# Optimization experiments

Measured on AMD Instinct MI355X. Metric: run time of the kernel, lower is better.

The kernel has to match this reference:

```python
import jax, jax.numpy as jnp
import numpy as np

N = 100000
E = 1600000
D_IN = 128
H = 128
C = 3
EPS_BN = 1e-5
EPS_LN = 1e-5


def _gcn_conv(x, W, b, src, dst, ew, n):
    # PyG GCNConv: x' = D^{-1/2} (A + I) D^{-1/2} (x W) + b, self-loop weight 1
    x = x @ W
    loop = jnp.arange(n)
    src2 = jnp.concatenate([src, loop])
    dst2 = jnp.concatenate([dst, loop])
    ew2 = jnp.concatenate([ew, jnp.ones((n,), dtype=x.dtype)])
    deg = jax.ops.segment_sum(ew2, dst2, num_segments=n)
    dinv = jnp.where(deg > 0, jax.lax.rsqrt(jnp.maximum(deg, 1e-12)), 0.0)
    norm = dinv[src2] * ew2 * dinv[dst2]  # [E+N]
    msgs = x[src2] * norm[:, None]        # [E+N, H] gathered messages
    out = jax.ops.segment_sum(msgs, dst2, num_segments=n)
    return out + b


def setup_inputs() -> dict:
    key = jax.random.key(0)
    ks = jax.random.split(key, 16)
    def lin(k, i, o):
        s = 1.0 / np.sqrt(i)
        k1, k2 = jax.random.split(k)
        return (jax.random.uniform(k1, (i, o), jnp.float32, -s, s),
                jax.random.uniform(k2, (o,), jnp.float32, -s, s))
    x = jax.random.normal(ks[0], (N, D_IN), jnp.float32)
    edge_index = jax.random.randint(ks[1], (2, E), 0, N, jnp.int64)
    edge_attr = jax.random.uniform(ks[2], (E, 1), jnp.float32)
    W_pre, b_pre = lin(ks[3], D_IN, H)
    W1, b1 = lin(ks[4], H, H)
    W2, b2 = lin(ks[5], H, H)
    Wc1, bc1 = lin(ks[6], H, H)
    Wc2, bc2 = lin(ks[7], H, C)
    return {
        "x": x, "edge_index": edge_index, "edge_attr": edge_attr,
        "W_pre": W_pre, "b_pre": b_pre,
        "bn_gamma": jnp.ones((H,), jnp.float32), "bn_beta": jnp.zeros((H,), jnp.float32),
        "bn_mean": jnp.zeros((H,), jnp.float32), "bn_var": jnp.ones((H,), jnp.float32),
        "W1": W1, "b1": b1, "W2": W2, "b2": b2,
        "Wc1": Wc1, "bc1": bc1,
        "ln_g": jnp.ones((H,), jnp.float32), "ln_b": jnp.zeros((H,), jnp.float32),
        "Wc2": Wc2, "bc2": bc2,
    }


def reference(x, edge_index, edge_attr, W_pre, b_pre, bn_gamma, bn_beta, bn_mean, bn_var,
              W1, b1, W2, b2, Wc1, bc1, ln_g, ln_b, Wc2, bc2):
    src, dst = edge_index[0], edge_index[1]
    ew = edge_attr.squeeze()
    n = x.shape[0]
    # input_preprocess: Linear -> BatchNorm1d (eval: running stats) -> ReLU (dropout=identity)
    h = x @ W_pre + b_pre
    h = (h - bn_mean) * jax.lax.rsqrt(bn_var + EPS_BN) * bn_gamma + bn_beta
    h = jax.nn.relu(h)
    residual = h
    # conv layer 1 (+ ReLU, dropout identity in eval)
    h = jax.nn.relu(_gcn_conv(h, W1, b1, src, dst, ew, n))
    # conv layer 2 (last: no activation)
    h = _gcn_conv(h, W2, b2, src, dst, ew, n)
    h = h + residual  # shapes match
    # classifier: Linear -> LayerNorm -> ReLU -> (dropout) -> Linear
    z = h @ Wc1 + bc1
    mu = jnp.mean(z, axis=-1, keepdims=True)
    var = jnp.mean((z - mu) ** 2, axis=-1, keepdims=True)
    z = (z - mu) * jax.lax.rsqrt(var + EPS_LN) * ln_g + ln_b
    z = jax.nn.relu(z)
    return z @ Wc2 + bc2
```

## Files before the change

### kernel.cpp

```cpp
#include <hip/hip_runtime.h>
#include <hip/hip_bf16.h>

typedef __bf16 bf16_t;
typedef bf16_t bf16x8 __attribute__((ext_vector_type(8)));
typedef float f32x4 __attribute__((ext_vector_type(4)));
typedef float f32x2 __attribute__((ext_vector_type(2)));

#define EPS_BN 1e-5f
#define EPS_LN 1e-5f
#define SLOTS 32
#define WSCALE 32767.f
#define WINV (1.f / 32767.f)
#define RNODES 448
#define OV_CAP 16384
#define OVA_CAP 65536

__device__ __forceinline__ float blo(unsigned u) { return __uint_as_float(u << 16); }
__device__ __forceinline__ float bhi(unsigned u) { return __uint_as_float(u & 0xFFFF0000u); }
__device__ __forceinline__ f32x2 f8lo(unsigned u) { return __builtin_amdgcn_cvt_pk_f32_fp8((int)u, false); }
__device__ __forceinline__ f32x2 f8hi(unsigned u) { return __builtin_amdgcn_cvt_pk_f32_fp8((int)u, true); }

#define ACC8(U, W) do { \
    f32x2 Wv = (f32x2){(W), (W)}; \
    acc[0] += Wv * f8lo((U).x); acc[1] += Wv * f8hi((U).x); \
    acc[2] += Wv * f8lo((U).y); acc[3] += Wv * f8hi((U).y); \
    acc[4] += Wv * f8lo((U).z); acc[5] += Wv * f8hi((U).z); \
    acc[6] += Wv * f8lo((U).w); acc[7] += Wv * f8hi((U).w); } while (0)


__global__ void prepK(const float* __restrict__ W0, const float* __restrict__ W1,
                      const float* __restrict__ W2, const float* __restrict__ W3,
                      bf16_t* __restrict__ WT, int* __restrict__ bCnt,
                      int* __restrict__ ovCnt, int* __restrict__ ovACnt) {
    int flat = blockIdx.x * 256 + threadIdx.x;
    if (flat == 0) { *ovCnt = 0; *ovACnt = 0; }
    if (flat < 4096) bCnt[flat] = 0;
    if (flat < 65536) {
        int which = flat >> 14, r = flat & 16383;
        const float* W = (which == 0) ? W0 : (which == 1) ? W1 : (which == 2) ? W2 : W3;
        int i = r >> 7, o = r & 127;
        WT[which * 128 * 136 + o * 136 + i] = (bf16_t)W[r];
    }
}


__global__ __launch_bounds__(256) void binK(
    const int* __restrict__ ei, const float* __restrict__ ea,
    uint2* __restrict__ bbuf, int* __restrict__ bCnt,
    uint2* __restrict__ ovA, int* __restrict__ ovACnt,
    int E, int cap, int nbuck)
{
    __shared__ int lcnt[256];
    __shared__ int gbase[256];
    int tid = threadIdx.x;

    for (int round = 0; round < 2; ++round) {
        if (tid < nbuck) lcnt[tid] = 0;
        __syncthreads();

        int e0 = blockIdx.x * 8192 + round * 4096 + tid;
        int d[16]; unsigned pk[16]; int p[16];
#pragma unroll
        for (int k = 0; k < 16; ++k) {
            int e = e0 + k * 256;
            p[k] = -1;
            if (e < E) {
                d[k] = ei[E + e];
                int s = ei[e];
                unsigned wq = __float2uint_rn(ea[e] * WSCALE);
                pk[k] = ((unsigned)s << 15) | wq;
                p[k] = atomicAdd(&lcnt[(unsigned)d[k] / RNODES], 1);
            }
        }
        __syncthreads();
        if (tid < nbuck) gbase[tid] = atomicAdd(&bCnt[tid * 16], lcnt[tid]);
        __syncthreads();
#pragma unroll
        for (int k = 0; k < 16; ++k) {
            if (p[k] >= 0) {
                int b = (unsigned)d[k] / RNODES;
                int idx = gbase[b] + p[k];
                if (idx < cap) {
                    bbuf[(size_t)b * cap + idx] = make_uint2((unsigned)d[k], pk[k]);
                } else {
                    int o = atomicAdd(ovACnt, 1);
                    if (o < OVA_CAP) ovA[o] = make_uint2((unsigned)d[k], pk[k]);
                }
            }
        }
        __syncthreads();
    }
}


__global__ __launch_bounds__(256) void buildK(
    const uint2* __restrict__ bbuf, const int* __restrict__ bCnt,
    const uint2* __restrict__ ovA, const int* __restrict__ ovACnt,
    unsigned* __restrict__ slots, int* __restrict__ cnt, float* __restrict__ dinv,
    uint2* __restrict__ ov, int* __restrict__ ovCnt,
    int cap, int n)
{
    __shared__ unsigned slotsL[RNODES * 32];
    __shared__ int cntL[RNODES];
    __shared__ float wsumL[RNODES];
    int tid = threadIdx.x;
    int base = blockIdx.x * RNODES;

    for (int j = tid; j < RNODES; j += 256) { cntL[j] = 0; wsumL[j] = 0.f; }
    __syncthreads();

    int nb = min(bCnt[blockIdx.x * 16], cap);
    const uint2* buf = bbuf + (size_t)blockIdx.x * cap;
    for (int i = tid; i < nb; i += 256) {
        uint2 u = buf[i];
        int local = (int)u.x - base;
        int pos = atomicAdd(&cntL[local], 1);
        atomicAdd(&wsumL[local], (float)(u.y & 32767u) * WINV);
        if (pos < SLOTS) {
            slotsL[local * 32 + pos] = u.y;
        } else {
            int o = atomicAdd(ovCnt, 1);
            if (o < OV_CAP) ov[o] = u;
        }
    }
    int no = min(*ovACnt, OVA_CAP);
    for (int k = tid; k < no; k += 256) {
        uint2 u = ovA[k];
        int local = (int)u.x - base;
        if (local >= 0 && local < RNODES) {
            int pos = atomicAdd(&cntL[local], 1);
            atomicAdd(&wsumL[local], (float)(u.y & 32767u) * WINV);
            if (pos < SLOTS) {
                slotsL[local * 32 + pos] = u.y;
            } else {
                int o = atomicAdd(ovCnt, 1);
                if (o < OV_CAP) ov[o] = u;
            }
        }
    }
    __syncthreads();

    for (int j = tid; j < RNODES; j += 256) {
        int node = base + j;
        if (node < n) {
            int c = cntL[j];
            int cm = min(c, SLOTS);
            int c8 = (cm + 7) & ~7;
            for (int k2 = cm; k2 < c8; ++k2) slotsL[j * 32 + k2] = (unsigned)node << 15;
            cnt[node] = c;
            dinv[node] = rsqrtf(fmaxf(1.f + wsumL[j], 1e-12f));
        }
    }
    __syncthreads();

    int vnodes = min(n - base, RNODES);
    if (vnodes <= 0) return;
    const uint4* sl4 = (const uint4*)slotsL;
    uint4* sg4 = (uint4*)(slots + ((size_t)base << 5));
    int lim = vnodes * 8;
    for (int i = tid; i < lim; i += 256) sg4[i] = sl4[i];
}


template <int MODE, typename AT>
__global__ __launch_bounds__(256) void gemm128K(
    const AT* __restrict__ A, const bf16_t* __restrict__ WT,
    bf16_t* __restrict__ outb, unsigned* __restrict__ out8,
    const float* __restrict__ colBias,
    const float* __restrict__ bnMean, const float* __restrict__ bnVar,
    const float* __restrict__ bnG, const float* __restrict__ bnB,
    const float* __restrict__ dinv, int nrows)
{
    __shared__ __align__(16) bf16_t Bs[128 * 136];
    int tid = threadIdx.x;
    int rb = blockIdx.x * 64;

    {
        const uint4* src = (const uint4*)WT;
        uint4* dst = (uint4*)Bs;
        if (MODE == 1) {
            for (int i = tid; i < 128 * 17; i += 256) {
                int row = i / 17, k = i - row * 17;
                int so = ((row & 15) << 3) | (row >> 4);
                dst[row * 17 + k] = src[so * 17 + k];
            }
        } else {
            for (int i = tid; i < 128 * 17; i += 256) dst[i] = src[i];
        }
    }

    int lane = tid & 63;
    int wid = tid >> 6;
    int m = lane & 15, q = lane >> 4;
    int myRow = rb + wid * 16 + m;
    int rowL = min(myRow, nrows - 1);

    bf16x8 af[4];
    if constexpr (sizeof(AT) == 4) {
#pragma unroll
        for (int kk = 0; kk < 4; ++kk) {
            float4 v0 = ((const float4*)A)[rowL * 32 + q * 2 + kk * 8];
            float4 v1 = ((const float4*)A)[rowL * 32 + q * 2 + kk * 8 + 1];
            bf16x8 w8;
            w8[0] = (bf16_t)v0.x; w8[1] = (bf16_t)v0.y; w8[2] = (bf16_t)v0.z; w8[3] = (bf16_t)v0.w;
            w8[4] = (bf16_t)v1.x; w8[5] = (bf16_t)v1.y; w8[6] = (bf16_t)v1.z; w8[7] = (bf16_t)v1.w;
            af[kk] = w8;
        }
    } else {
#pragma unroll
        for (int kk = 0; kk < 4; ++kk)
            af[kk] = ((const bf16x8*)A)[rowL * 16 + q + kk * 4];
    }

    __syncthreads();

    f32x4 acc[8];
#pragma unroll
    for (int c = 0; c < 8; ++c) acc[c] = (f32x4){0.f, 0.f, 0.f, 0.f};

#pragma unroll
    for (int kk = 0; kk < 4; ++kk) {
#pragma unroll
        for (int c = 0; c < 8; ++c) {
            bf16x8 bfr = *(const bf16x8*)&Bs[(c * 16 + m) * 136 + q * 8 + kk * 32];
            acc[c] = __builtin_amdgcn_mfma_f32_16x16x32_bf16(af[kk], bfr, acc[c], 0, 0, 0);
        }
    }

    int r0 = rb + wid * 16 + q * 4;
    if (MODE == 1) {
        float dv[4];
#pragma unroll
        for (int i = 0; i < 4; ++i) dv[i] = (r0 + i < nrows) ? dinv[r0 + i] : 0.f;
#pragma unroll
        for (int i = 0; i < 4; ++i) {
            int r = r0 + i;
            if (r < nrows) {
                float v0 = acc[0][i] * dv[i], v1 = acc[1][i] * dv[i];
                float v2 = acc[2][i] * dv[i], v3 = acc[3][i] * dv[i];
                float v4 = acc[4][i] * dv[i], v5 = acc[5][i] * dv[i];
                float v6 = acc[6][i] * dv[i], v7 = acc[7][i] * dv[i];
                int lo = __builtin_amdgcn_cvt_pk_fp8_f32(v0, v1, 0, false);
                lo = __builtin_amdgcn_cvt_pk_fp8_f32(v2, v3, lo, true);
                int hi = __builtin_amdgcn_cvt_pk_fp8_f32(v4, v5, 0, false);
                hi = __builtin_amdgcn_cvt_pk_fp8_f32(v6, v7, hi, true);
                ((uint2*)out8)[(r << 4) | m] = make_uint2((unsigned)lo, (unsigned)hi);
            }
        }
    } else {
#pragma unroll
        for (int c = 0; c < 8; ++c) {
            int j = c * 16 + m;
            float cb = colBias[j];
            float rs = rsqrtf(bnVar[j] + EPS_BN);
            float scale = bnG[j] * rs;
            float shift = bnB[j] - bnMean[j] * scale;
#pragma unroll
            for (int i = 0; i < 4; ++i) {
                int r = r0 + i;
                if (r < nrows) {
                    float v = (acc[c][i] + cb) * scale + shift;
                    outb[r * 128 + j] = (bf16_t)fmaxf(v, 0.f);
                }
            }
        }
    }
}


template <int RELU, int RES>
__global__ __launch_bounds__(256) void aggK(
    const uint4* __restrict__ ts16, const unsigned* __restrict__ slots,
    const int* __restrict__ cnt, const float* __restrict__ dinv,
    const float4* __restrict__ bias, const uint4* __restrict__ residual,
    uint4* __restrict__ out,
    const uint2* __restrict__ ov, const int* __restrict__ ovCnt, int n)
{
    int tid = threadIdx.x;
    int node = blockIdx.x * 8 + (tid >> 5);
    int hl = tid & 31;
    int hb = tid & 32;
    if (node >= n) return;
    int slot = hl >> 3;
    int f = hl & 7;
    int nb = node << 5;

    int c8 = (min(cnt[node], SLOTS) + 7) & ~7;
    unsigned my = slots[nb | hl];
    float myw = (float)(my & 32767u) * WINV;
    int myoff = (int)(my >> 15) << 3;

    f32x2 acc[8];
#pragma unroll
    for (int k = 0; k < 8; ++k) acc[k] = (f32x2){0.f, 0.f};

    if (slot == 1) {
        uint4 su = ts16[(node << 3) + f];
        acc[0] += f8lo(su.x); acc[1] += f8hi(su.x);
        acc[2] += f8lo(su.y); acc[3] += f8hi(su.y);
        acc[4] += f8lo(su.z); acc[5] += f8hi(su.z);
        acc[6] += f8lo(su.w); acc[7] += f8hi(su.w);
    }

    for (int j = 0; j < c8; j += 8) {
        int s0 = hb + j + slot;
        int s1 = s0 + 4;
        int o0 = __shfl(myoff, s0);
        int o1 = __shfl(myoff, s1);
        float w0 = __shfl(myw, s0);
        float w1 = __shfl(myw, s1);
        uint4 u0 = ts16[o0 + f];
        uint4 u1 = ts16[o1 + f];
        ACC8(u0, w0);
        ACC8(u1, w1);
    }

    int no = min(*ovCnt, OV_CAP);
    for (int k = 0; k < no; ++k) {
        uint2 o = ov[k];
        if ((int)o.x == node && slot == 0) {
            uint4 u = ts16[((int)(o.y >> 15) << 3) + f];
            float w = (float)(o.y & 32767u) * WINV;
            ACC8(u, w);
        }
    }

#pragma unroll
    for (int k = 0; k < 8; ++k) {
        f32x2 t;
        t.x = __shfl_xor(acc[k].x, 8);  t.y = __shfl_xor(acc[k].y, 8);
        acc[k] += t;
        t.x = __shfl_xor(acc[k].x, 16); t.y = __shfl_xor(acc[k].y, 16);
        acc[k] += t;
    }

    if (slot == 0) {
        float di = dinv[node];
        float r[16];
#pragma unroll
        for (int k = 0; k < 8; ++k) {
            float4 bb = bias[f * 4 + (k >> 1)];
            float b0 = (k & 1) ? bb.z : bb.x;
            float b1 = (k & 1) ? bb.w : bb.y;
            r[2 * k]     = acc[k].x * di + b0;
            r[2 * k + 1] = acc[k].y * di + b1;
        }
        if (RES) {
            uint4 q0 = residual[(node << 4) + f * 2];
            uint4 q1 = residual[(node << 4) + f * 2 + 1];
            r[0] += blo(q0.x);  r[1] += bhi(q0.x);
            r[2] += blo(q0.y);  r[3] += bhi(q0.y);
            r[4] += blo(q0.z);  r[5] += bhi(q0.z);
            r[6] += blo(q0.w);  r[7] += bhi(q0.w);
            r[8] += blo(q1.x);  r[9] += bhi(q1.x);
            r[10] += blo(q1.y); r[11] += bhi(q1.y);
            r[12] += blo(q1.z); r[13] += bhi(q1.z);
            r[14] += blo(q1.w); r[15] += bhi(q1.w);
        }
        if (RELU) {
#pragma unroll
            for (int k = 0; k < 16; ++k) r[k] = fmaxf(r[k], 0.f);
        }
        bf16x8 o0, o1;
#pragma unroll
        for (int k = 0; k < 8; ++k) { o0[k] = (bf16_t)r[k]; o1[k] = (bf16_t)r[8 + k]; }
        out[(node << 4) + f * 2]     = *(uint4*)&o0;
        out[(node << 4) + f * 2 + 1] = *(uint4*)&o1;
    }
}


__global__ __launch_bounds__(256) void classifierK(
    const bf16_t* __restrict__ A, const bf16_t* __restrict__ WT,
    const float* __restrict__ bc1, const float* __restrict__ g,
    const float* __restrict__ b, const float* __restrict__ Wc2,
    const float* __restrict__ bc2, float* __restrict__ out, int nrows)
{
    __shared__ __align__(16) bf16_t Bs[128 * 136];
    __shared__ float sB[128], sG[128], sLb[128], sW2[384];
    int tid = threadIdx.x;
    int rb = blockIdx.x * 64;

    {
        const uint4* src = (const uint4*)WT;
        uint4* dst = (uint4*)Bs;
        for (int i = tid; i < 128 * 17; i += 256) dst[i] = src[i];
    }
    if (tid < 128) { sB[tid] = bc1[tid]; sG[tid] = g[tid]; sLb[tid] = b[tid]; }
    for (int i = tid; i < 384; i += 256) sW2[i] = Wc2[i];

    int lane = tid & 63;
    int wid = tid >> 6;
    int m = lane & 15, q = lane >> 4;
    int rowL = min(rb + wid * 16 + m, nrows - 1);

    bf16x8 af[4];
#pragma unroll
    for (int kk = 0; kk < 4; ++kk)
        af[kk] = ((const bf16x8*)A)[rowL * 16 + q + kk * 4];

    __syncthreads();

    f32x4 acc[8];
#pragma unroll
    for (int c = 0; c < 8; ++c) acc[c] = (f32x4){0.f, 0.f, 0.f, 0.f};
#pragma unroll
    for (int kk = 0; kk < 4; ++kk) {
#pragma unroll
        for (int c = 0; c < 8; ++c) {
            bf16x8 bfr = *(const bf16x8*)&Bs[(c * 16 + m) * 136 + q * 8 + kk * 32];
            acc[c] = __builtin_amdgcn_mfma_f32_16x16x32_bf16(af[kk], bfr, acc[c], 0, 0, 0);
        }
    }

    int r0 = rb + wid * 16 + q * 4;
#pragma unroll
    for (int i = 0; i < 4; ++i) {
        float s1 = 0.f, s2 = 0.f;
#pragma unroll
        for (int c = 0; c < 8; ++c) {
            float z = acc[c][i] + sB[c * 16 + m];
            acc[c][i] = z;
            s1 += z; s2 += z * z;
        }
#pragma unroll
        for (int off = 1; off < 16; off <<= 1) {
            s1 += __shfl_xor(s1, off);
            s2 += __shfl_xor(s2, off);
        }
        float mu = s1 * (1.f / 128.f);
        float var = s2 * (1.f / 128.f) - mu * mu;
        float rstd = rsqrtf(var + EPS_LN);
        float p0 = 0.f, p1 = 0.f, p2 = 0.f;
#pragma unroll
        for (int c = 0; c < 8; ++c) {
            int j = c * 16 + m;
            float zn = (acc[c][i] - mu) * rstd * sG[j] + sLb[j];
            zn = fmaxf(zn, 0.f);
            p0 += zn * sW2[j * 3 + 0];
            p1 += zn * sW2[j * 3 + 1];
            p2 += zn * sW2[j * 3 + 2];
        }
#pragma unroll
        for (int off = 1; off < 16; off <<= 1) {
            p0 += __shfl_xor(p0, off);
            p1 += __shfl_xor(p1, off);
            p2 += __shfl_xor(p2, off);
        }
        int r = r0 + i;
        if (m == 0 && r < nrows) {
            out[r * 3 + 0] = p0 + bc2[0];
            out[r * 3 + 1] = p1 + bc2[1];
            out[r * 3 + 2] = p2 + bc2[2];
        }
    }
}


extern "C" void kernel_launch(void* const* d_in, const int* in_sizes, int n_in,
                              void* d_out, int out_size, void* d_ws, size_t ws_size,
                              hipStream_t stream) {
    const float* x      = (const float*)d_in[0];
    const int*   ei     = (const int*)d_in[1];
    const float* ea     = (const float*)d_in[2];
    const float* W_pre  = (const float*)d_in[3];
    const float* b_pre  = (const float*)d_in[4];
    const float* bn_g   = (const float*)d_in[5];
    const float* bn_b   = (const float*)d_in[6];
    const float* bn_m   = (const float*)d_in[7];
    const float* bn_v   = (const float*)d_in[8];
    const float* W1     = (const float*)d_in[9];
    const float* b1     = (const float*)d_in[10];
    const float* W2     = (const float*)d_in[11];
    const float* b2     = (const float*)d_in[12];
    const float* Wc1    = (const float*)d_in[13];
    const float* bc1    = (const float*)d_in[14];
    const float* ln_g   = (const float*)d_in[15];
    const float* ln_b   = (const float*)d_in[16];
    const float* Wc2    = (const float*)d_in[17];
    const float* bc2    = (const float*)d_in[18];
    float* outp = (float*)d_out;

    const int N = in_sizes[0] / 128;
    const int E = in_sizes[2];

    char* p = (char*)d_ws;
    auto alloc = [&](size_t bytes) -> void* {
        void* r = (void*)p;
        p += (bytes + 255) & ~(size_t)255;
        return r;
    };
    bf16_t*   h0    = (bf16_t*)alloc((size_t)N * 128 * 2);
    bf16_t*   bufB  = (bf16_t*)alloc((size_t)N * 128 * 2);
    unsigned* ts8   = (unsigned*)alloc((size_t)N * 128);
    float*    dinv  = (float*)alloc((size_t)N * 4);
    int*      cnt   = (int*)alloc((size_t)N * 4);
    int*      ovCnt = (int*)alloc(256);
    int*      ovACnt= (int*)alloc(256);
    uint2*    ov    = (uint2*)alloc((size_t)OV_CAP * 8);
    uint2*    ovA   = (uint2*)alloc((size_t)OVA_CAP * 8);
    unsigned* slots = (unsigned*)alloc((size_t)N * SLOTS * 4);
    bf16_t*   WT    = (bf16_t*)alloc((size_t)4 * 128 * 136 * 2);
    int       nbuck = (N + RNODES - 1) / RNODES;
    int       cap   = E / nbuck + 4096;
    uint2*    bbuf  = (uint2*)alloc((size_t)nbuck * cap * 8);
    int*      bCnt  = (int*)alloc(4096 * 4);

    bf16_t* WT_pre = WT + 0 * 128 * 136;
    bf16_t* WT_1   = WT + 1 * 128 * 136;
    bf16_t* WT_2   = WT + 2 * 128 * 136;
    bf16_t* WT_c1  = WT + 3 * 128 * 136;

    int gG = (N + 63) / 64;
    int gH = (N + 7) / 8;
    int gP = 65536 / 256;
    int gBin = (E + 8191) / 8192;

    prepK<<<gP, 256, 0, stream>>>(W_pre, W1, W2, Wc1, WT, bCnt, ovCnt, ovACnt);
    binK<<<gBin, 256, 0, stream>>>(ei, ea, bbuf, bCnt, ovA, ovACnt, E, cap, nbuck);
    buildK<<<nbuck, 256, 0, stream>>>(bbuf, bCnt, ovA, ovACnt, slots, cnt, dinv, ov, ovCnt, cap, N);

    gemm128K<0, float><<<gG, 256, 0, stream>>>(x, WT_pre, h0, nullptr, b_pre, bn_m, bn_v, bn_g, bn_b, nullptr, N);
    gemm128K<1, bf16_t><<<gG, 256, 0, stream>>>(h0, WT_1, nullptr, ts8, nullptr, nullptr, nullptr, nullptr, nullptr, dinv, N);
    aggK<1, 0><<<gH, 256, 0, stream>>>((const uint4*)ts8, slots, cnt, dinv, (const float4*)b1,
                                       nullptr, (uint4*)bufB, ov, ovCnt, N);
    gemm128K<1, bf16_t><<<gG, 256, 0, stream>>>(bufB, WT_2, nullptr, ts8, nullptr, nullptr, nullptr, nullptr, nullptr, dinv, N);
    aggK<0, 1><<<gH, 256, 0, stream>>>((const uint4*)ts8, slots, cnt, dinv, (const float4*)b2,
                                       (const uint4*)h0, (uint4*)bufB, ov, ovCnt, N);
    classifierK<<<gG, 256, 0, stream>>>(bufB, WT_c1, bc1, ln_g, ln_b, Wc2, bc2, outp, N);
}
```

Baseline: 325.4 us.

## Split aggregation feature dimension across paired blocks and halve edge-binning work per block

```diff
diff --git a/kernel.cpp b/kernel.cpp
--- a/kernel.cpp
+++ b/kernel.cpp
@@ -53,42 +53,38 @@
     __shared__ int lcnt[256];
     __shared__ int gbase[256];
     int tid = threadIdx.x;
-
-    for (int round = 0; round < 2; ++round) {
-        if (tid < nbuck) lcnt[tid] = 0;
-        __syncthreads();
-
-        int e0 = blockIdx.x * 8192 + round * 4096 + tid;
-        int d[16]; unsigned pk[16]; int p[16];
-#pragma unroll
-        for (int k = 0; k < 16; ++k) {
-            int e = e0 + k * 256;
-            p[k] = -1;
-            if (e < E) {
-                d[k] = ei[E + e];
-                int s = ei[e];
-                unsigned wq = __float2uint_rn(ea[e] * WSCALE);
-                pk[k] = ((unsigned)s << 15) | wq;
-                p[k] = atomicAdd(&lcnt[(unsigned)d[k] / RNODES], 1);
+    if (tid < nbuck) lcnt[tid] = 0;
+    __syncthreads();
+
+    int e0 = blockIdx.x * 4096 + tid;
+    int d[16]; unsigned pk[16]; int p[16];
+#pragma unroll
+    for (int k = 0; k < 16; ++k) {
+        int e = e0 + k * 256;
+        p[k] = -1;
+        if (e < E) {
+            d[k] = ei[E + e];
+            int s = ei[e];
+            unsigned wq = __float2uint_rn(ea[e] * WSCALE);
+            pk[k] = ((unsigned)s << 15) | wq;
+            p[k] = atomicAdd(&lcnt[(unsigned)d[k] / RNODES], 1);
+        }
+    }
+    __syncthreads();
+    if (tid < nbuck) gbase[tid] = atomicAdd(&bCnt[tid * 16], lcnt[tid]);
+    __syncthreads();
+#pragma unroll
+    for (int k = 0; k < 16; ++k) {
+        if (p[k] >= 0) {
+            int b = (unsigned)d[k] / RNODES;
+            int idx = gbase[b] + p[k];
+            if (idx < cap) {
+                bbuf[(size_t)b * cap + idx] = make_uint2((unsigned)d[k], pk[k]);
+            } else {
+                int o = atomicAdd(ovACnt, 1);
+                if (o < OVA_CAP) ovA[o] = make_uint2((unsigned)d[k], pk[k]);
             }
         }
-        __syncthreads();
-        if (tid < nbuck) gbase[tid] = atomicAdd(&bCnt[tid * 16], lcnt[tid]);
-        __syncthreads();
-#pragma unroll
-        for (int k = 0; k < 16; ++k) {
-            if (p[k] >= 0) {
-                int b = (unsigned)d[k] / RNODES;
-                int idx = gbase[b] + p[k];
-                if (idx < cap) {
-                    bbuf[(size_t)b * cap + idx] = make_uint2((unsigned)d[k], pk[k]);
-                } else {
-                    int o = atomicAdd(ovACnt, 1);
-                    if (o < OVA_CAP) ovA[o] = make_uint2((unsigned)d[k], pk[k]);
-                }
-            }
-        }
-        __syncthreads();
     }
 }
 
@@ -269,7 +265,7 @@
 
 
 template <int RELU, int RES>
-__global__ __launch_bounds__(256) void aggK(
+__global__ __launch_bounds__(256) void aggHK(
     const uint4* __restrict__ ts16, const unsigned* __restrict__ slots,
     const int* __restrict__ cnt, const float* __restrict__ dinv,
     const float4* __restrict__ bias, const uint4* __restrict__ residual,
@@ -277,16 +273,18 @@
     const uint2* __restrict__ ov, const int* __restrict__ ovCnt, int n)
 {
     int tid = threadIdx.x;
-    int node = blockIdx.x * 8 + (tid >> 5);
+    int b = blockIdx.x;
+    int p = (b >> 2) & 1;
+    int g = ((b >> 3) << 2) | (b & 3);
+    int node = g * 8 + (tid >> 5);
     int hl = tid & 31;
     int hb = tid & 32;
     if (node >= n) return;
-    int slot = hl >> 3;
-    int f = hl & 7;
-    int nb = node << 5;
+    int slot = hl >> 2;
+    int fc = (p << 2) | (hl & 3);
 
     int c8 = (min(cnt[node], SLOTS) + 7) & ~7;
-    unsigned my = slots[nb | hl];
+    unsigned my = slots[(node << 5) | hl];
     float myw = (float)(my & 32767u) * WINV;
     int myoff = (int)(my >> 15) << 3;
 
@@ -295,7 +293,7 @@
     for (int k = 0; k < 8; ++k) acc[k] = (f32x2){0.f, 0.f};
 
     if (slot == 1) {
-        uint4 su = ts16[(node << 3) + f];
+        uint4 su = ts16[(node << 3) + fc];
         acc[0] += f8lo(su.x); acc[1] += f8hi(su.x);
         acc[2] += f8lo(su.y); acc[3] += f8hi(su.y);
         acc[4] += f8lo(su.z); acc[5] += f8hi(su.z);
@@ -304,22 +302,17 @@
 
     for (int j = 0; j < c8; j += 8) {
         int s0 = hb + j + slot;
-        int s1 = s0 + 4;
         int o0 = __shfl(myoff, s0);
-        int o1 = __shfl(myoff, s1);
         float w0 = __shfl(myw, s0);
-        float w1 = __shfl(myw, s1);
-        uint4 u0 = ts16[o0 + f];
-        uint4 u1 = ts16[o1 + f];
+        uint4 u0 = ts16[o0 + fc];
         ACC8(u0, w0);
-        ACC8(u1, w1);
     }
 
     int no = min(*ovCnt, OV_CAP);
     for (int k = 0; k < no; ++k) {
         uint2 o = ov[k];
         if ((int)o.x == node && slot == 0) {
-            uint4 u = ts16[((int)(o.y >> 15) << 3) + f];
+            uint4 u = ts16[((int)(o.y >> 15) << 3) + fc];
             float w = (float)(o.y & 32767u) * WINV;
             ACC8(u, w);
         }
@@ -328,10 +321,9 @@
 #pragma unroll
     for (int k = 0; k < 8; ++k) {
         f32x2 t;
-        t.x = __shfl_xor(acc[k].x, 8);  t.y = __shfl_xor(acc[k].y, 8);
-        acc[k] += t;
-        t.x = __shfl_xor(acc[k].x, 16); t.y = __shfl_xor(acc[k].y, 16);
-        acc[k] += t;
+        t.x = __shfl_xor(acc[k].x, 4);  t.y = __shfl_xor(acc[k].y, 4);  acc[k] += t;
+        t.x = __shfl_xor(acc[k].x, 8);  t.y = __shfl_xor(acc[k].y, 8);  acc[k] += t;
+        t.x = __shfl_xor(acc[k].x, 16); t.y = __shfl_xor(acc[k].y, 16); acc[k] += t;
     }
 
     if (slot == 0) {
@@ -339,15 +331,15 @@
         float r[16];
 #pragma unroll
         for (int k = 0; k < 8; ++k) {
-            float4 bb = bias[f * 4 + (k >> 1)];
+            float4 bb = bias[fc * 4 + (k >> 1)];
             float b0 = (k & 1) ? bb.z : bb.x;
             float b1 = (k & 1) ? bb.w : bb.y;
             r[2 * k]     = acc[k].x * di + b0;
             r[2 * k + 1] = acc[k].y * di + b1;
         }
         if (RES) {
-            uint4 q0 = residual[(node << 4) + f * 2];
-            uint4 q1 = residual[(node << 4) + f * 2 + 1];
+            uint4 q0 = residual[(node << 4) + fc * 2];
+            uint4 q1 = residual[(node << 4) + fc * 2 + 1];
             r[0] += blo(q0.x);  r[1] += bhi(q0.x);
             r[2] += blo(q0.y);  r[3] += bhi(q0.y);
             r[4] += blo(q0.z);  r[5] += bhi(q0.z);
@@ -364,8 +356,8 @@
         bf16x8 o0, o1;
 #pragma unroll
         for (int k = 0; k < 8; ++k) { o0[k] = (bf16_t)r[k]; o1[k] = (bf16_t)r[8 + k]; }
-        out[(node << 4) + f * 2]     = *(uint4*)&o0;
-        out[(node << 4) + f * 2 + 1] = *(uint4*)&o1;
+        out[(node << 4) + fc * 2]     = *(uint4*)&o0;
+        out[(node << 4) + fc * 2 + 1] = *(uint4*)&o1;
     }
 }
 
@@ -512,9 +504,10 @@
     bf16_t* WT_c1  = WT + 3 * 128 * 136;
 
     int gG = (N + 63) / 64;
-    int gH = (N + 7) / 8;
+    int nGrp = (N + 7) / 8;
+    int gAgg = ((nGrp + 3) / 4) * 8;
     int gP = 65536 / 256;
-    int gBin = (E + 8191) / 8192;
+    int gBin = (E + 4095) / 4096;
 
     prepK<<<gP, 256, 0, stream>>>(W_pre, W1, W2, Wc1, WT, bCnt, ovCnt, ovACnt);
     binK<<<gBin, 256, 0, stream>>>(ei, ea, bbuf, bCnt, ovA, ovACnt, E, cap, nbuck);
@@ -522,10 +515,10 @@
 
     gemm128K<0, float><<<gG, 256, 0, stream>>>(x, WT_pre, h0, nullptr, b_pre, bn_m, bn_v, bn_g, bn_b, nullptr, N);
     gemm128K<1, bf16_t><<<gG, 256, 0, stream>>>(h0, WT_1, nullptr, ts8, nullptr, nullptr, nullptr, nullptr, nullptr, dinv, N);
-    aggK<1, 0><<<gH, 256, 0, stream>>>((const uint4*)ts8, slots, cnt, dinv, (const float4*)b1,
-                                       nullptr, (uint4*)bufB, ov, ovCnt, N);
+    aggHK<1, 0><<<gAgg, 256, 0, stream>>>((const uint4*)ts8, slots, cnt, dinv, (const float4*)b1,
+                                          nullptr, (uint4*)bufB, ov, ovCnt, N);
     gemm128K<1, bf16_t><<<gG, 256, 0, stream>>>(bufB, WT_2, nullptr, ts8, nullptr, nullptr, nullptr, nullptr, nullptr, dinv, N);
-    aggK<0, 1><<<gH, 256, 0, stream>>>((const uint4*)ts8, slots, cnt, dinv, (const float4*)b2,
-                                       (const uint4*)h0, (uint4*)bufB, ov, ovCnt, N);
+    aggHK<0, 1><<<gAgg, 256, 0, stream>>>((const uint4*)ts8, slots, cnt, dinv, (const float4*)b2,
+                                          (const uint4*)h0, (uint4*)bufB, ov, ovCnt, N);
     classifierK<<<gG, 256, 0, stream>>>(bufB, WT_c1, bc1, ln_g, ln_b, Wc2, bc2, outp, N);
 }
```

New measurement: 390.0 us. 1.2x slower.

## Fuse preprocess GEMM with first conv GEMM and halve binning block size

Applied to the files above, without the earlier changes.

```diff
diff --git a/kernel.cpp b/kernel.cpp
--- a/kernel.cpp
+++ b/kernel.cpp
@@ -53,42 +53,38 @@
     __shared__ int lcnt[256];
     __shared__ int gbase[256];
     int tid = threadIdx.x;
-
-    for (int round = 0; round < 2; ++round) {
-        if (tid < nbuck) lcnt[tid] = 0;
-        __syncthreads();
-
-        int e0 = blockIdx.x * 8192 + round * 4096 + tid;
-        int d[16]; unsigned pk[16]; int p[16];
-#pragma unroll
-        for (int k = 0; k < 16; ++k) {
-            int e = e0 + k * 256;
-            p[k] = -1;
-            if (e < E) {
-                d[k] = ei[E + e];
-                int s = ei[e];
-                unsigned wq = __float2uint_rn(ea[e] * WSCALE);
-                pk[k] = ((unsigned)s << 15) | wq;
-                p[k] = atomicAdd(&lcnt[(unsigned)d[k] / RNODES], 1);
+    if (tid < nbuck) lcnt[tid] = 0;
+    __syncthreads();
+
+    int e0 = blockIdx.x * 4096 + tid;
+    int d[16]; unsigned pk[16]; int p[16];
+#pragma unroll
+    for (int k = 0; k < 16; ++k) {
+        int e = e0 + k * 256;
+        p[k] = -1;
+        if (e < E) {
+            d[k] = ei[E + e];
+            int s = ei[e];
+            unsigned wq = __float2uint_rn(ea[e] * WSCALE);
+            pk[k] = ((unsigned)s << 15) | wq;
+            p[k] = atomicAdd(&lcnt[(unsigned)d[k] / RNODES], 1);
+        }
+    }
+    __syncthreads();
+    if (tid < nbuck) gbase[tid] = atomicAdd(&bCnt[tid * 16], lcnt[tid]);
+    __syncthreads();
+#pragma unroll
+    for (int k = 0; k < 16; ++k) {
+        if (p[k] >= 0) {
+            int b = (unsigned)d[k] / RNODES;
+            int idx = gbase[b] + p[k];
+            if (idx < cap) {
+                bbuf[(size_t)b * cap + idx] = make_uint2((unsigned)d[k], pk[k]);
+            } else {
+                int o = atomicAdd(ovACnt, 1);
+                if (o < OVA_CAP) ovA[o] = make_uint2((unsigned)d[k], pk[k]);
             }
         }
-        __syncthreads();
-        if (tid < nbuck) gbase[tid] = atomicAdd(&bCnt[tid * 16], lcnt[tid]);
-        __syncthreads();
-#pragma unroll
-        for (int k = 0; k < 16; ++k) {
-            if (p[k] >= 0) {
-                int b = (unsigned)d[k] / RNODES;
-                int idx = gbase[b] + p[k];
-                if (idx < cap) {
-                    bbuf[(size_t)b * cap + idx] = make_uint2((unsigned)d[k], pk[k]);
-                } else {
-                    int o = atomicAdd(ovACnt, 1);
-                    if (o < OVA_CAP) ovA[o] = make_uint2((unsigned)d[k], pk[k]);
-                }
-            }
-        }
-        __syncthreads();
     }
 }
 
@@ -162,13 +158,124 @@
 }
 
 
+__device__ __forceinline__ void stageB512(const bf16_t* __restrict__ WT, bf16_t* __restrict__ Bs,
+                                          int tid) {
+    const uint4* src = (const uint4*)WT;
+    uint4* dst = (uint4*)Bs;
+    for (int i = tid; i < 128 * 17; i += 512) {
+        int row = i / 17, k = i - row * 17;
+        int so = ((row & 15) << 3) | (row >> 4);
+        dst[row * 17 + k] = src[so * 17 + k];
+    }
+}
+
+__device__ __forceinline__ void mfma128(const bf16_t* __restrict__ Bs, const bf16x8* af,
+                                        f32x4* acc, int m, int q) {
+#pragma unroll
+    for (int kk = 0; kk < 4; ++kk) {
+#pragma unroll
+        for (int c = 0; c < 8; ++c) {
+            bf16x8 bfr = *(const bf16x8*)&Bs[(c * 16 + m) * 136 + q * 8 + kk * 32];
+            acc[c] = __builtin_amdgcn_mfma_f32_16x16x32_bf16(af[kk], bfr, acc[c], 0, 0, 0);
+        }
+    }
+}
+
+__global__ __launch_bounds__(512) void fusePreK(
+    const float* __restrict__ x, const bf16_t* __restrict__ WTpre, const bf16_t* __restrict__ WT1,
+    bf16_t* __restrict__ h0, unsigned* __restrict__ ts8,
+    const float* __restrict__ b_pre,
+    const float* __restrict__ bnMean, const float* __restrict__ bnVar,
+    const float* __restrict__ bnG, const float* __restrict__ bnB,
+    const float* __restrict__ dinv, int n)
+{
+    __shared__ __align__(16) bf16_t U[128 * 136];
+    int tid = threadIdx.x;
+    int rb = blockIdx.x * 128;
+    int lane = tid & 63, wid = tid >> 6;
+    int m = lane & 15, q = lane >> 4;
+
+    stageB512(WTpre, U, tid);
+
+    float scale[8], shift[8];
+#pragma unroll
+    for (int c = 0; c < 8; ++c) {
+        int j = m * 8 + c;
+        float rs = rsqrtf(bnVar[j] + EPS_BN);
+        scale[c] = bnG[j] * rs;
+        shift[c] = bnB[j] - bnMean[j] * scale[c] + b_pre[j] * scale[c];
+    }
+
+    int rowL = min(rb + wid * 16 + m, n - 1);
+    bf16x8 af[4];
+#pragma unroll
+    for (int kk = 0; kk < 4; ++kk) {
+        float4 v0 = ((const float4*)x)[rowL * 32 + q * 2 + kk * 8];
+        float4 v1 = ((const float4*)x)[rowL * 32 + q * 2 + kk * 8 + 1];
+        bf16x8 w8;
+        w8[0] = (bf16_t)v0.x; w8[1] = (bf16_t)v0.y; w8[2] = (bf16_t)v0.z; w8[3] = (bf16_t)v0.w;
+        w8[4] = (bf16_t)v1.x; w8[5] = (bf16_t)v1.y; w8[6] = (bf16_t)v1.z; w8[7] = (bf16_t)v1.w;
+        af[kk] = w8;
+    }
+    __syncthreads();
+
+    f32x4 acc[8];
+#pragma unroll
+    for (int c = 0; c < 8; ++c) acc[c] = (f32x4){0.f, 0.f, 0.f, 0.f};
+    mfma128(U, af, acc, m, q);
+    __syncthreads();
+
+    int r0 = rb + wid * 16 + q * 4;
+#pragma unroll
+    for (int i = 0; i < 4; ++i) {
+        bf16x8 hv;
+#pragma unroll
+        for (int c = 0; c < 8; ++c)
+            hv[c] = (bf16_t)fmaxf(acc[c][i] * scale[c] + shift[c], 0.f);
+        int lr = wid * 16 + q * 4 + i;
+        *(uint4*)&U[lr * 136 + m * 8] = *(uint4*)&hv;
+        int r = r0 + i;
+        if (r < n) ((uint4*)h0)[r * 16 + m] = *(uint4*)&hv;
+    }
+    __syncthreads();
+
+    int lrow = min(wid * 16 + m, 127);
+#pragma unroll
+    for (int kk = 0; kk < 4; ++kk)
+        af[kk] = *(const bf16x8*)&U[lrow * 136 + q * 8 + kk * 32];
+    __syncthreads();
+    stageB512(WT1, U, tid);
+    __syncthreads();
+
+#pragma unroll
+    for (int c = 0; c < 8; ++c) acc[c] = (f32x4){0.f, 0.f, 0.f, 0.f};
+    mfma128(U, af, acc, m, q);
+
+    float dv[4];
+#pragma unroll
+    for (int i = 0; i < 4; ++i) dv[i] = (r0 + i < n) ? dinv[r0 + i] : 0.f;
+#pragma unroll
+    for (int i = 0; i < 4; ++i) {
+        int r = r0 + i;
+        if (r < n) {
+            float v0 = acc[0][i] * dv[i], v1 = acc[1][i] * dv[i];
+            float v2 = acc[2][i] * dv[i], v3 = acc[3][i] * dv[i];
+            float v4 = acc[4][i] * dv[i], v5 = acc[5][i] * dv[i];
+            float v6 = acc[6][i] * dv[i], v7 = acc[7][i] * dv[i];
+            int lo = __builtin_amdgcn_cvt_pk_fp8_f32(v0, v1, 0, false);
+            lo = __builtin_amdgcn_cvt_pk_fp8_f32(v2, v3, lo, true);
+            int hi = __builtin_amdgcn_cvt_pk_fp8_f32(v4, v5, 0, false);
+            hi = __builtin_amdgcn_cvt_pk_fp8_f32(v6, v7, hi, true);
+            ((uint2*)ts8)[(r << 4) | m] = make_uint2((unsigned)lo, (unsigned)hi);
+        }
+    }
+}
+
+
 template <int MODE, typename AT>
 __global__ __launch_bounds__(256) void gemm128K(
     const AT* __restrict__ A, const bf16_t* __restrict__ WT,
     bf16_t* __restrict__ outb, unsigned* __restrict__ out8,
-    const float* __restrict__ colBias,
-    const float* __restrict__ bnMean, const float* __restrict__ bnVar,
-    const float* __restrict__ bnG, const float* __restrict__ bnB,
     const float* __restrict__ dinv, int nrows)
 {
     __shared__ __align__(16) bf16_t Bs[128 * 136];
@@ -178,39 +285,22 @@
     {
         const uint4* src = (const uint4*)WT;
         uint4* dst = (uint4*)Bs;
-        if (MODE == 1) {
-            for (int i = tid; i < 128 * 17; i += 256) {
-                int row = i / 17, k = i - row * 17;
-                int so = ((row & 15) << 3) | (row >> 4);
-                dst[row * 17 + k] = src[so * 17 + k];
-            }
-        } else {
-            for (int i = tid; i < 128 * 17; i += 256) dst[i] = src[i];
+        for (int i = tid; i < 128 * 17; i += 256) {
+            int row = i / 17, k = i - row * 17;
+            int so = ((row & 15) << 3) | (row >> 4);
+            dst[row * 17 + k] = src[so * 17 + k];
         }
     }
 
     int lane = tid & 63;
     int wid = tid >> 6;
     int m = lane & 15, q = lane >> 4;
-    int myRow = rb + wid * 16 + m;
-    int rowL = min(myRow, nrows - 1);
+    int rowL = min(rb + wid * 16 + m, nrows - 1);
 
     bf16x8 af[4];
-    if constexpr (sizeof(AT) == 4) {
-#pragma unroll
-        for (int kk = 0; kk < 4; ++kk) {
-            float4 v0 = ((const float4*)A)[rowL * 32 + q * 2 + kk * 8];
-            float4 v1 = ((const float4*)A)[rowL * 32 + q * 2 + kk * 8 + 1];
-            bf16x8 w8;
-            w8[0] = (bf16_t)v0.x; w8[1] = (bf16_t)v0.y; w8[2] = (bf16_t)v0.z; w8[3] = (bf16_t)v0.w;
-            w8[4] = (bf16_t)v1.x; w8[5] = (bf16_t)v1.y; w8[6] = (bf16_t)v1.z; w8[7] = (bf16_t)v1.w;
-            af[kk] = w8;
-        }
-    } else {
-#pragma unroll
-        for (int kk = 0; kk < 4; ++kk)
-            af[kk] = ((const bf16x8*)A)[rowL * 16 + q + kk * 4];
-    }
+#pragma unroll
+    for (int kk = 0; kk < 4; ++kk)
+        af[kk] = ((const bf16x8*)A)[rowL * 16 + q + kk * 4];
 
     __syncthreads();
 
@@ -228,41 +318,22 @@
     }
 
     int r0 = rb + wid * 16 + q * 4;
-    if (MODE == 1) {
-        float dv[4];
-#pragma unroll
-        for (int i = 0; i < 4; ++i) dv[i] = (r0 + i < nrows) ? dinv[r0 + i] : 0.f;
-#pragma unroll
-        for (int i = 0; i < 4; ++i) {
-            int r = r0 + i;
-            if (r < nrows) {
-                float v0 = acc[0][i] * dv[i], v1 = acc[1][i] * dv[i];
-                float v2 = acc[2][i] * dv[i], v3 = acc[3][i] * dv[i];
-                float v4 = acc[4][i] * dv[i], v5 = acc[5][i] * dv[i];
-                float v6 = acc[6][i] * dv[i], v7 = acc[7][i] * dv[i];
-                int lo = __builtin_amdgcn_cvt_pk_fp8_f32(v0, v1, 0, false);
-                lo = __builtin_amdgcn_cvt_pk_fp8_f32(v2, v3, lo, true);
-                int hi = __builtin_amdgcn_cvt_pk_fp8_f32(v4, v5, 0, false);
-                hi = __builtin_amdgcn_cvt_pk_fp8_f32(v6, v7, hi, true);
-                ((uint2*)out8)[(r << 4) | m] = make_uint2((unsigned)lo, (unsigned)hi);
-            }
-        }
-    } else {
-#pragma unroll
-        for (int c = 0; c < 8; ++c) {
-            int j = c * 16 + m;
-            float cb = colBias[j];
-            float rs = rsqrtf(bnVar[j] + EPS_BN);
-            float scale = bnG[j] * rs;
-            float shift = bnB[j] - bnMean[j] * scale;
-#pragma unroll
-            for (int i = 0; i < 4; ++i) {
-                int r = r0 + i;
-                if (r < nrows) {
-                    float v = (acc[c][i] + cb) * scale + shift;
-                    outb[r * 128 + j] = (bf16_t)fmaxf(v, 0.f);
-                }
-            }
+    float dv[4];
+#pragma unroll
+    for (int i = 0; i < 4; ++i) dv[i] = (r0 + i < nrows) ? dinv[r0 + i] : 0.f;
+#pragma unroll
+    for (int i = 0; i < 4; ++i) {
+        int r = r0 + i;
+        if (r < nrows) {
+            float v0 = acc[0][i] * dv[i], v1 = acc[1][i] * dv[i];
+            float v2 = acc[2][i] * dv[i], v3 = acc[3][i] * dv[i];
+            float v4 = acc[4][i] * dv[i], v5 = acc[5][i] * dv[i];
+            float v6 = acc[6][i] * dv[i], v7 = acc[7][i] * dv[i];
+            int lo = __builtin_amdgcn_cvt_pk_fp8_f32(v0, v1, 0, false);
+            lo = __builtin_amdgcn_cvt_pk_fp8_f32(v2, v3, lo, true);
+            int hi = __builtin_amdgcn_cvt_pk_fp8_f32(v4, v5, 0, false);
+            hi = __builtin_amdgcn_cvt_pk_fp8_f32(v6, v7, hi, true);
+            ((uint2*)out8)[(r << 4) | m] = make_uint2((unsigned)lo, (unsigned)hi);
         }
     }
 }
@@ -512,19 +583,19 @@
     bf16_t* WT_c1  = WT + 3 * 128 * 136;
 
     int gG = (N + 63) / 64;
+    int gF = (N + 127) / 128;
     int gH = (N + 7) / 8;
     int gP = 65536 / 256;
-    int gBin = (E + 8191) / 8192;
+    int gBin = (E + 4095) / 4096;
 
     prepK<<<gP, 256, 0, stream>>>(W_pre, W1, W2, Wc1, WT, bCnt, ovCnt, ovACnt);
     binK<<<gBin, 256, 0, stream>>>(ei, ea, bbuf, bCnt, ovA, ovACnt, E, cap, nbuck);
     buildK<<<nbuck, 256, 0, stream>>>(bbuf, bCnt, ovA, ovACnt, slots, cnt, dinv, ov, ovCnt, cap, N);
 
-    gemm128K<0, float><<<gG, 256, 0, stream>>>(x, WT_pre, h0, nullptr, b_pre, bn_m, bn_v, bn_g, bn_b, nullptr, N);
-    gemm128K<1, bf16_t><<<gG, 256, 0, stream>>>(h0, WT_1, nullptr, ts8, nullptr, nullptr, nullptr, nullptr, nullptr, dinv, N);
+    fusePreK<<<gF, 512, 0, stream>>>(x, WT_pre, WT_1, h0, ts8, b_pre, bn_m, bn_v, bn_g, bn_b, dinv, N);
     aggK<1, 0><<<gH, 256, 0, stream>>>((const uint4*)ts8, slots, cnt, dinv, (const float4*)b1,
                                        nullptr, (uint4*)bufB, ov, ovCnt, N);
-    gemm128K<1, bf16_t><<<gG, 256, 0, stream>>>(bufB, WT_2, nullptr, ts8, nullptr, nullptr, nullptr, nullptr, nullptr, dinv, N);
+    gemm128K<1, bf16_t><<<gG, 256, 0, stream>>>(bufB, WT_2, nullptr, ts8, dinv, N);
     aggK<0, 1><<<gH, 256, 0, stream>>>((const uint4*)ts8, slots, cnt, dinv, (const float4*)b2,
                                        (const uint4*)h0, (uint4*)bufB, ov, ovCnt, N);
     classifierK<<<gG, 256, 0, stream>>>(bufB, WT_c1, bc1, ln_g, ln_b, Wc2, bc2, outp, N);
```

Result: faster. 314.9 us (-3.2%).
